# Kernel tuning notes

Measured on AMD Instinct MI355X. Metric: run time of the kernel, lower is better.

The kernel has to match this reference:

```python
import jax, jax.numpy as jnp
import numpy as np


def setup_inputs() -> dict:
    key = jax.random.key(0)
    k1, k2, k3 = jax.random.split(key, 3)
    B, S, E = 2, 2048, 2048
    H, O, A = 16, 1024, 128  # heads, codebook options, head_size (E = H*A)
    x = jax.random.normal(k1, (B, S, E), dtype=jnp.float32)
    vq_head_weights = jax.random.normal(k2, (H, O, A), dtype=jnp.float32) * 0.02
    vq_codebooks = jax.random.normal(k3, (H, O, A), dtype=jnp.float32) * 0.02
    temperature = jnp.ones((1,), dtype=jnp.float32)
    return {"x": x, "vq_head_weights": vq_head_weights, "vq_codebooks": vq_codebooks, "temperature": temperature}


def reference(x, vq_head_weights, vq_codebooks, temperature):
    # Training-mode, frozen, use_temperature=True path (straight-through VQ):
    # probs = one_hot(argmax(logits)) + softmax(logits/T) - stop_grad(softmax(logits/T))
    B, S, E = x.shape
    H, O, A = vq_head_weights.shape
    x_prepped = x.reshape(B, S, H, A)
    logits = jnp.einsum('bsha,hoa->bsho', x_prepped, vq_head_weights)
    probs = jax.nn.softmax(logits / temperature[0], axis=-1)
    argmax = jnp.argmax(logits, axis=-1)  # [B,S,H]
    hard_probs = jax.nn.one_hot(argmax, O, dtype=logits.dtype)
    probs = hard_probs + probs - jax.lax.stop_gradient(probs)
    out = jnp.einsum('bsho,hoa->bsha', probs, vq_codebooks)
    return out.reshape(B, S, E)
```

## Files before the change

kernel.cpp:

```cpp
#include <hip/hip_runtime.h>

typedef _Float16 half8 __attribute__((ext_vector_type(8)));
typedef float    f32x16 __attribute__((ext_vector_type(16)));

constexpr int kH = 16;
constexpr int kO = 1024;
constexpr int kA = 128;
constexpr int kBS = 4096;
constexpr int MTILE = 64;
constexpr int NITER = 16;

__global__ void split_w(const float* __restrict__ w, ushort* __restrict__ wp) {
    int idx  = blockIdx.x * 256 + threadIdx.x;
    int l31  = idx & 31;
    int half = (idx >> 5) & 1;
    int ks   = (idx >> 6) & 7;
    int t    = (idx >> 9) & 31;
    int h    = idx >> 14;
    const float* src = w + ((h * kO + t * 32 + l31) * kA) + ks * 16 + half * 8;
    float4 v0 = *(const float4*)(src);
    float4 v1 = *(const float4*)(src + 4);
    float va[8] = { v0.x, v0.y, v0.z, v0.w, v1.x, v1.y, v1.z, v1.w };
    ushort hh[8], ll[8];
#pragma unroll
    for (int j = 0; j < 8; ++j) {
        _Float16 hj = (_Float16)va[j];
        _Float16 lj = (_Float16)(va[j] - (float)hj);
        hh[j] = __builtin_bit_cast(ushort, hj);
        ll[j] = __builtin_bit_cast(ushort, lj);
    }
    ushort4 hv0 = { hh[0], hh[1], hh[2], hh[3] }, hv1 = { hh[4], hh[5], hh[6], hh[7] };
    ushort4 lv0 = { ll[0], ll[1], ll[2], ll[3] }, lv1 = { ll[4], ll[5], ll[6], ll[7] };
    int lane = half * 32 + l31;
    ushort* dhi = wp + (h * 32 + t) * 8192 + ks * 512 + lane * 8;
    *(ushort4*)(dhi)        = hv0;
    *(ushort4*)(dhi + 4)    = hv1;
    *(ushort4*)(dhi + 4096) = lv0;
    *(ushort4*)(dhi + 4100) = lv1;
}

__launch_bounds__(256, 4)
__global__ void vq_argmax_gather(const float* __restrict__ x,
                                 const ushort* __restrict__ wp,
                                 const float* __restrict__ cb,
                                 float* __restrict__ out) {
    __shared__ float red_max[2][MTILE];
    __shared__ int   red_idx[2][MTILE];

    const int tid   = threadIdx.x;
    const int lane  = tid & 63;
    const int wv    = tid >> 6;
    const int nhalf = wv >> 1;
    const int mtile = wv & 1;
    const int bid   = blockIdx.x;
    const int h  = ((bid & 7) << 1) | ((bid >> 3) & 1);
    const int p0 = (bid >> 4) * MTILE;

    const int l31  = lane & 31;
    const int half = lane >> 5;

    const ushort* wbase = wp + (h * 32 + nhalf * 16) * 8192 + lane * 8;

    uint4 wreg[8];
    auto loadW = [&](int it, int plane) {
        const ushort* p = wbase + it * 8192 + plane * 4096;
#pragma unroll
        for (int ks = 0; ks < 8; ++ks)
            wreg[ks] = *(const uint4*)(p + ks * 512);
    };

    loadW(0, 0);

    const int mrow = p0 + mtile * 32 + l31;
    const float* xbase = x + (mrow * kH + h) * kA + half * 8;
    half8 xh[8], xl[8];
#pragma unroll
    for (int ks = 0; ks < 8; ++ks) {
        float4 v0 = *(const float4*)(xbase + ks * 16);
        float4 v1 = *(const float4*)(xbase + ks * 16 + 4);
        float va[8] = { v0.x, v0.y, v0.z, v0.w, v1.x, v1.y, v1.z, v1.w };
        half8 hi, lo;
#pragma unroll
        for (int j = 0; j < 8; ++j) {
            _Float16 hj = (_Float16)va[j];
            hi[j] = hj;
            lo[j] = (_Float16)(va[j] - (float)hj);
        }
        xh[ks] = hi; xl[ks] = lo;
    }

    float best = -1e30f;
    int   bidx = 0;
    const int nwb = nhalf * (kO / 2);

    for (int it = 0; it < NITER; ++it) {
        f32x16 acc = {};
#pragma unroll
        for (int ks = 0; ks < 8; ++ks)
            acc = __builtin_amdgcn_mfma_f32_32x32x16_f16(
                __builtin_bit_cast(half8, wreg[ks]), xh[ks], acc, 0, 0, 0);
#pragma unroll
        for (int ks = 0; ks < 8; ++ks)
            acc = __builtin_amdgcn_mfma_f32_32x32x16_f16(
                __builtin_bit_cast(half8, wreg[ks]), xl[ks], acc, 0, 0, 0);
        loadW(it, 1);
#pragma unroll
        for (int ks = 0; ks < 8; ++ks)
            acc = __builtin_amdgcn_mfma_f32_32x32x16_f16(
                __builtin_bit_cast(half8, wreg[ks]), xh[ks], acc, 0, 0, 0);
        if (it + 1 < NITER) loadW(it + 1, 0);

        float lv = acc[0];
        int   lr = 0;
#pragma unroll
        for (int r = 1; r < 16; ++r) {
            if (acc[r] > lv) { lv = acc[r]; lr = r; }
        }
        int li = nwb + it * 32 + 4 * half + (lr & 3) + 8 * (lr >> 2);
        if (lv > best) { best = lv; bidx = li; }
    }

    {
        float om = __shfl_xor(best, 32, 64);
        int   oi = __shfl_xor(bidx, 32, 64);
        if (om > best || (om == best && oi < bidx)) { best = om; bidx = oi; }
    }
    if (half == 0) {
        red_max[nhalf][mtile * 32 + l31] = best;
        red_idx[nhalf][mtile * 32 + l31] = bidx;
    }
    __syncthreads();

    for (int i = tid; i < MTILE * 32; i += 256) {
        int row = i >> 5, ch = i & 31;
        float m0 = red_max[0][row], m1 = red_max[1][row];
        int o = (m1 > m0) ? red_idx[1][row] : red_idx[0][row];
        float4 v = *(const float4*)(cb + (h * kO + o) * kA + ch * 4);
        *(float4*)(out + ((p0 + row) * kH + h) * kA + ch * 4) = v;
    }
}

extern "C" void kernel_launch(void* const* d_in, const int* in_sizes, int n_in,
                              void* d_out, int out_size, void* d_ws, size_t ws_size,
                              hipStream_t stream) {
    const float* x  = (const float*)d_in[0];
    const float* w  = (const float*)d_in[1];
    const float* cb = (const float*)d_in[2];
    float* out = (float*)d_out;

    ushort* wpacked = (ushort*)d_ws;

    split_w<<<dim3(1024), dim3(256), 0, stream>>>(w, wpacked);
    vq_argmax_gather<<<dim3((kBS / MTILE) * kH), dim3(256), 0, stream>>>(x, wpacked, cb, out);
}
```

Baseline: 153.2 us.

## Double-buffer full weight tiles in registers and coalesce split_w reads

The main kernel now loads both hi and lo weight planes for a whole tile into one of two register buffers and ping-pongs between them, so the next tile's loads are issued while the current tile's MFMAs run. Launch bounds drop from 4 to 2 waves per SIMD to make room for the larger register footprint. The preprocessing kernel is rewritten so each wave reads contiguous float2 rows of the weights, giving coalesced reads at the cost of narrower scattered stores. The trade is lower occupancy against deeper per-wave load prefetch.

```diff
diff --git a/kernel.cpp b/kernel.cpp
--- a/kernel.cpp
+++ b/kernel.cpp
@@ -11,35 +11,27 @@
 constexpr int NITER = 16;
 
 __global__ void split_w(const float* __restrict__ w, ushort* __restrict__ wp) {
-    int idx  = blockIdx.x * 256 + threadIdx.x;
-    int l31  = idx & 31;
-    int half = (idx >> 5) & 1;
-    int ks   = (idx >> 6) & 7;
-    int t    = (idx >> 9) & 31;
-    int h    = idx >> 14;
-    const float* src = w + ((h * kO + t * 32 + l31) * kA) + ks * 16 + half * 8;
-    float4 v0 = *(const float4*)(src);
-    float4 v1 = *(const float4*)(src + 4);
-    float va[8] = { v0.x, v0.y, v0.z, v0.w, v1.x, v1.y, v1.z, v1.w };
-    ushort hh[8], ll[8];
+    const int lane = threadIdx.x & 63;
+    const int gw   = blockIdx.x * 4 + (threadIdx.x >> 6);
+    const int ks   = lane >> 3;
+    const int half = (lane >> 2) & 1;
+    const int j    = (2 * lane) & 7;
 #pragma unroll
-    for (int j = 0; j < 8; ++j) {
-        _Float16 hj = (_Float16)va[j];
-        _Float16 lj = (_Float16)(va[j] - (float)hj);
-        hh[j] = __builtin_bit_cast(ushort, hj);
-        ll[j] = __builtin_bit_cast(ushort, lj);
+    for (int q = 0; q < 4; ++q) {
+        int r = gw * 4 + q;
+        int h = r >> 10, o = r & 1023, t = o >> 5, o31 = o & 31;
+        float2 v = *(const float2*)(w + r * kA + lane * 2);
+        _Float16 h0 = (_Float16)v.x, h1 = (_Float16)v.y;
+        _Float16 l0 = (_Float16)(v.x - (float)h0), l1 = (_Float16)(v.y - (float)h1);
+        ushort2 hv = { __builtin_bit_cast(ushort, h0), __builtin_bit_cast(ushort, h1) };
+        ushort2 lv = { __builtin_bit_cast(ushort, l0), __builtin_bit_cast(ushort, l1) };
+        ushort* d = wp + (h * 32 + t) * 8192 + ks * 512 + (half * 32 + o31) * 8 + j;
+        *(ushort2*)d = hv;
+        *(ushort2*)(d + 4096) = lv;
     }
-    ushort4 hv0 = { hh[0], hh[1], hh[2], hh[3] }, hv1 = { hh[4], hh[5], hh[6], hh[7] };
-    ushort4 lv0 = { ll[0], ll[1], ll[2], ll[3] }, lv1 = { ll[4], ll[5], ll[6], ll[7] };
-    int lane = half * 32 + l31;
-    ushort* dhi = wp + (h * 32 + t) * 8192 + ks * 512 + lane * 8;
-    *(ushort4*)(dhi)        = hv0;
-    *(ushort4*)(dhi + 4)    = hv1;
-    *(ushort4*)(dhi + 4096) = lv0;
-    *(ushort4*)(dhi + 4100) = lv1;
 }
 
-__launch_bounds__(256, 4)
+__launch_bounds__(256, 2)
 __global__ void vq_argmax_gather(const float* __restrict__ x,
                                  const ushort* __restrict__ wp,
                                  const float* __restrict__ cb,
@@ -61,15 +53,17 @@
 
     const ushort* wbase = wp + (h * 32 + nhalf * 16) * 8192 + lane * 8;
 
-    uint4 wreg[8];
-    auto loadW = [&](int it, int plane) {
-        const ushort* p = wbase + it * 8192 + plane * 4096;
+    uint4 bufA[16], bufB[16];
+    auto loadTile = [&](uint4* buf, int it) {
+        const ushort* p = wbase + it * 8192;
 #pragma unroll
-        for (int ks = 0; ks < 8; ++ks)
-            wreg[ks] = *(const uint4*)(p + ks * 512);
+        for (int ks = 0; ks < 8; ++ks) {
+            buf[ks]     = *(const uint4*)(p + ks * 512);
+            buf[8 + ks] = *(const uint4*)(p + 4096 + ks * 512);
+        }
     };
 
-    loadW(0, 0);
+    loadTile(bufA, 0);
 
     const int mrow = p0 + mtile * 32 + l31;
     const float* xbase = x + (mrow * kH + h) * kA + half * 8;
@@ -93,23 +87,20 @@
     int   bidx = 0;
     const int nwb = nhalf * (kO / 2);
 
-    for (int it = 0; it < NITER; ++it) {
+    auto computeTile = [&](const uint4* buf, int it) {
         f32x16 acc = {};
 #pragma unroll
         for (int ks = 0; ks < 8; ++ks)
             acc = __builtin_amdgcn_mfma_f32_32x32x16_f16(
-                __builtin_bit_cast(half8, wreg[ks]), xh[ks], acc, 0, 0, 0);
+                __builtin_bit_cast(half8, buf[ks]), xh[ks], acc, 0, 0, 0);
 #pragma unroll
         for (int ks = 0; ks < 8; ++ks)
             acc = __builtin_amdgcn_mfma_f32_32x32x16_f16(
-                __builtin_bit_cast(half8, wreg[ks]), xl[ks], acc, 0, 0, 0);
-        loadW(it, 1);
+                __builtin_bit_cast(half8, buf[ks]), xl[ks], acc, 0, 0, 0);
 #pragma unroll
         for (int ks = 0; ks < 8; ++ks)
             acc = __builtin_amdgcn_mfma_f32_32x32x16_f16(
-                __builtin_bit_cast(half8, wreg[ks]), xh[ks], acc, 0, 0, 0);
-        if (it + 1 < NITER) loadW(it + 1, 0);
-
+                __builtin_bit_cast(half8, buf[8 + ks]), xh[ks], acc, 0, 0, 0);
         float lv = acc[0];
         int   lr = 0;
 #pragma unroll
@@ -118,6 +109,13 @@
         }
         int li = nwb + it * 32 + 4 * half + (lr & 3) + 8 * (lr >> 2);
         if (lv > best) { best = lv; bidx = li; }
+    };
+
+    for (int it2 = 0; it2 < NITER; it2 += 2) {
+        loadTile(bufB, it2 + 1);
+        computeTile(bufA, it2);
+        if (it2 + 2 < NITER) loadTile(bufA, it2 + 2);
+        computeTile(bufB, it2 + 1);
     }
 
     {
```

New measurement: 159.4 us. +4.0%, slower.
